# Kernel optimization log

Hardware: AMD Instinct MI355X
Metric: run time of the kernel (lower is better)

The kernel has to match this reference:

```python
import jax, jax.numpy as jnp
import numpy as np

N, C, H, W = 32, 512, 56, 56
L, CT, HEAD, GROUPS = 64, 512, 16, 16
SIZE, POS_DIM = 14, 49  # PosEncoder(size=14, num_downsample=1) -> 14^2 // 4 = 49


def setup_inputs() -> dict:
    key = jax.random.key(0)
    ks = jax.random.split(key, 8)
    return {
        "feature": jax.random.normal(ks[0], (N, C, H, W), jnp.float32),
        "w_tc": jax.random.normal(ks[1], (L, C), jnp.float32) * 0.02,
        "b_tc": jnp.zeros((L,), jnp.float32),
        "w_val": jax.random.normal(ks[2], (GROUPS, CT // GROUPS, C // GROUPS), jnp.float32) * 0.02,
        "b_val": jnp.zeros((CT,), jnp.float32),
        "w_ds3": jax.random.normal(ks[3], (1, 1, 3, 3), jnp.float32) * 0.1,
        "b_ds3": jnp.zeros((1,), jnp.float32),
        "w_ds1": jax.random.normal(ks[4], (1, 1), jnp.float32) * 0.1,
        "b_ds1": jnp.zeros((1,), jnp.float32),
        "w_pos": jax.random.normal(ks[5], (POS_DIM, POS_DIM), jnp.float32) * 0.02,
        "b_pos": jnp.zeros((POS_DIM,), jnp.float32),
        "w_tok": jax.random.normal(ks[6], (CT, CT + POS_DIM), jnp.float32) * 0.02,
        "b_tok": jnp.zeros((CT,), jnp.float32),
    }


def reference(feature, w_tc, b_tc, w_val, b_val, w_ds3, b_ds3, w_ds1, b_ds1,
              w_pos, b_pos, w_tok, b_tok):
    n, c, h, w = feature.shape
    hw = h * w
    # --- static token coefficients: 1x1 conv C->L, scale, softmax over HW ---
    tc = jnp.einsum('nchw,lc->nlhw', feature, w_tc) + b_tc[None, :, None, None]
    tc = tc.reshape(n, 1, L, hw).transpose(0, 1, 3, 2) / np.sqrt(c)  # (N,1,HW,L)
    tc = jax.nn.softmax(tc, axis=2)
    # --- grouped 1x1 conv value: C -> CT (groups=16) ---
    fg = feature.reshape(n, GROUPS, c // GROUPS, hw)
    val = jnp.einsum('ngci,gdc->ngdi', fg, w_val).reshape(n, CT, hw) + b_val[None, :, None]
    val = val.reshape(n, HEAD, CT // HEAD, hw)
    # --- token aggregation: (N,h,CT/h,HW) @ (N,1,HW,L) -> (N,CT,L) ---
    tokens = jnp.matmul(val, tc).reshape(n, CT, -1)
    # --- PosEncoder: view coef maps as images, nearest-resize to 14x14 ---
    pc = tc.reshape(n * L, 1, h, w)  # torch .view memory reinterpretation
    ih = (jnp.arange(SIZE) * h) // SIZE
    iw = (jnp.arange(SIZE) * w) // SIZE
    pc = pc[:, :, ih][:, :, :, iw]  # (N*L,1,14,14) nearest interpolate
    # conv3x3 stride 2 pad 1: 14 -> 7
    pc = jax.lax.conv_general_dilated(pc, w_ds3, (2, 2), ((1, 1), (1, 1))) + b_ds3[None, :, None, None]
    # conv1x1 (1->1)
    pc = jnp.einsum('nchw,dc->ndhw', pc, w_ds1) + b_ds1[None, :, None, None]
    pc = pc.reshape(n, L, POS_DIM).transpose(0, 2, 1)  # (N,49,L)
    pos = jnp.einsum('ncl,dc->ndl', pc, w_pos) + b_pos[None, :, None]
    # --- concat + final 1x1 conv1d (CT+49 -> CT) ---
    tokens = jnp.concatenate([tokens, pos], axis=1)
    tokens = jnp.einsum('ncl,dc->ndl', tokens, w_tok) + b_tok[None, :, None]
    return tokens  # (N, CT, L)
```

## Files before the change

### kernel.cpp

```cpp
#include <hip/hip_runtime.h>
#include <cstddef>
#include <cstdint>

namespace {

constexpr int kN = 32;
constexpr int kC = 512;
constexpr int kHW = 3136;
constexpr int kL = 64;
constexpr int kCT = 512;
constexpr int kTok = 561;
constexpr int kKcat = 576;

typedef float fx4 __attribute__((ext_vector_type(4)));
typedef float f32x4 __attribute__((ext_vector_type(4)));
typedef short short8 __attribute__((ext_vector_type(8)));
typedef unsigned int u32x2 __attribute__((ext_vector_type(2)));

static __device__ inline unsigned pack_bf16(float a, float b) {
  unsigned ua = __builtin_bit_cast(unsigned, a) + 0x8000u;
  unsigned ub = __builtin_bit_cast(unsigned, b) + 0x8000u;
  return __builtin_amdgcn_perm(ub, ua, 0x07060302u);
}

__global__ __launch_bounds__(256) void build_wcat_kernel(
    const float* __restrict__ w_tok, const float* __restrict__ w_val,
    float* __restrict__ wcat) {
  int idx = blockIdx.x * 256 + threadIdx.x;
  if (idx >= kCT * kKcat) return;
  int d = idx / kKcat;
  int c = idx - d * kKcat;
  float v = 0.f;
  if (c < kCT) {
    int g = c >> 5, k = c & 31;
    const float* wt = w_tok + (size_t)d * kTok + g * 32;
    const float* wv = w_val + g * 1024 + k;
    float s = 0.f;
#pragma unroll
    for (int dp = 0; dp < 32; ++dp) s += wt[dp] * wv[dp * 32];
    v = s;
  } else if (c < kTok) {
    v = w_tok[(size_t)d * kTok + c];
  }
  wcat[idx] = v;
}

__global__ __launch_bounds__(256) void build_cst_kernel(
    const float* __restrict__ w_tok, const float* __restrict__ b_val,
    const float* __restrict__ b_tok, float* __restrict__ cst) {
  int d = blockIdx.x * 256 + threadIdx.x;
  if (d >= kCT) return;
  float s = b_tok[d];
  for (int c = 0; c < kCT; ++c) s += w_tok[(size_t)d * kTok + c] * b_val[c];
  cst[d] = s;
}

__global__ __launch_bounds__(256) void zero_pad_kernel(float* __restrict__ bcat) {
  int i = blockIdx.x * 256 + threadIdx.x;
  const int tot = kN * kL * (kKcat - kTok);
  if (i >= tot) return;
  int n = i / (kL * 15);
  int r = i - n * (kL * 15);
  int l = r / 15;
  int k = kTok + (r - l * 15);
  bcat[(size_t)n * kL * kKcat + (size_t)l * kKcat + k] = 0.f;
}

__global__ __launch_bounds__(256) void tc_gemm_kernel(
    const float* __restrict__ feat, const float* __restrict__ w_tc,
    const float* __restrict__ b_tc, float* __restrict__ tcT) {
  const int n = blockIdx.y;
  const int pb = blockIdx.x * 256;
  const int tid = threadIdx.x;
  const int wave = tid >> 6, lane = tid & 63;
  const int quad = lane >> 4, l16 = lane & 15;
  __shared__ unsigned short As[64][72];
  __shared__ unsigned short Bs[256][72];
  __shared__ float bsm[64];
  if (tid < 64) bsm[tid] = b_tc[tid];

  f32x4 acc[4][4];
#pragma unroll
  for (int i = 0; i < 4; ++i)
#pragma unroll
    for (int j = 0; j < 4; ++j) acc[i][j] = (f32x4){0.f, 0.f, 0.f, 0.f};

  const float* fb = feat + (size_t)n * kC * kHW;
  const int al = tid & 63, akg = (tid >> 6) * 16;
  const int bc4 = (tid & 15) * 4, bpl0 = (tid >> 4) * 4;

  for (int c0 = 0; c0 < kC; c0 += 64) {
    const float* asrc = w_tc + (size_t)al * kC + c0 + akg;
#pragma unroll
    for (int u = 0; u < 4; ++u) {
      fx4 v = *(const fx4*)(asrc + u * 4);
      u32x2 w = {pack_bf16(v[0], v[1]), pack_bf16(v[2], v[3])};
      *(u32x2*)&As[al][akg + u * 4] = w;
    }
#pragma unroll
    for (int pass = 0; pass < 4; ++pass) {
      int pl = bpl0 + pass * 64;
      int pe = pb + pl;
      pe = pe < 3132 ? pe : 3132;
      fx4 v0 = *(const fx4*)(fb + (size_t)(c0 + bc4 + 0) * kHW + pe);
      fx4 v1 = *(const fx4*)(fb + (size_t)(c0 + bc4 + 1) * kHW + pe);
      fx4 v2 = *(const fx4*)(fb + (size_t)(c0 + bc4 + 2) * kHW + pe);
      fx4 v3 = *(const fx4*)(fb + (size_t)(c0 + bc4 + 3) * kHW + pe);
#pragma unroll
      for (int j = 0; j < 4; ++j) {
        u32x2 w = {pack_bf16(v0[j], v1[j]), pack_bf16(v2[j], v3[j])};
        *(u32x2*)&Bs[pl + j][bc4] = w;
      }
    }
    __syncthreads();
#pragma unroll
    for (int ks = 0; ks < 2; ++ks) {
      short8 a[4], b[4];
#pragma unroll
      for (int i = 0; i < 4; ++i)
        a[i] = *(const short8*)&As[i * 16 + l16][ks * 32 + quad * 8];
#pragma unroll
      for (int j = 0; j < 4; ++j)
        b[j] = *(const short8*)&Bs[wave * 64 + j * 16 + l16][ks * 32 + quad * 8];
#pragma unroll
      for (int i = 0; i < 4; ++i)
#pragma unroll
        for (int j = 0; j < 4; ++j)
          acc[i][j] = __builtin_amdgcn_mfma_f32_16x16x32_bf16(a[i], b[j], acc[i][j], 0, 0, 0);
    }
    __syncthreads();
  }

  const float inv = 0.04419417382415922f;
  float* ob = tcT + (size_t)n * kL * kHW;
#pragma unroll
  for (int ti = 0; ti < 4; ++ti) {
#pragma unroll
    for (int tj = 0; tj < 4; ++tj) {
      int pg = pb + wave * 64 + tj * 16 + l16;
      if (pg < kHW) {
#pragma unroll
        for (int r = 0; r < 4; ++r) {
          int l = ti * 16 + quad * 4 + r;
          ob[(size_t)l * kHW + pg] = (acc[ti][tj][r] + bsm[l]) * inv;
        }
      }
    }
  }
}

__global__ __launch_bounds__(256) void softmax_stats_kernel(
    const float* __restrict__ tcT, float* __restrict__ mArr,
    float* __restrict__ invArr) {
  const int row = blockIdx.x * 4 + (threadIdx.x >> 6);
  const int lane = threadIdx.x & 63;
  const float* src = tcT + (size_t)row * kHW + lane * 4;
  fx4 x[13];
#pragma unroll
  for (int i = 0; i < 12; ++i) x[i] = *(const fx4*)(src + i * 256);
  if (lane < 16)
    x[12] = *(const fx4*)(src + 3072);
  else
    x[12] = (fx4){-1e30f, -1e30f, -1e30f, -1e30f};
  float m = -1e30f;
#pragma unroll
  for (int i = 0; i < 13; ++i)
    m = fmaxf(m, fmaxf(fmaxf(x[i][0], x[i][1]), fmaxf(x[i][2], x[i][3])));
#pragma unroll
  for (int off = 32; off >= 1; off >>= 1) m = fmaxf(m, __shfl_xor(m, off));
  float s = 0.f;
#pragma unroll
  for (int i = 0; i < 13; ++i) {
    s += __expf(x[i][0] - m) + __expf(x[i][1] - m) + __expf(x[i][2] - m) +
         __expf(x[i][3] - m);
  }
#pragma unroll
  for (int off = 32; off >= 1; off >>= 1) s += __shfl_xor(s, off);
  if (lane == 0) {
    mArr[row] = m;
    invArr[row] = 1.f / s;
  }
}

__global__ __launch_bounds__(256) void m_gemm_kernel(
    const float* __restrict__ feat, const float* __restrict__ tcT,
    const float* __restrict__ mArr, const float* __restrict__ invArr,
    float* __restrict__ part, int klen) {
  const int cb = blockIdx.x * 256;
  const int n = blockIdx.y;
  const int s = blockIdx.z;
  const int p0s = s * klen;
  const int tid = threadIdx.x;
  const int wave = tid >> 6, lane = tid & 63;
  const int quad = lane >> 4, l16 = lane & 15;
  __shared__ unsigned short As[64][72];
  __shared__ unsigned short Bs[256][72];

  const int al = tid & 63, akg = (tid >> 6) * 16;
  const float sm = mArr[n * 64 + al];
  const float si = invArr[n * 64 + al];

  f32x4 acc[4][4];
#pragma unroll
  for (int i = 0; i < 4; ++i)
#pragma unroll
    for (int j = 0; j < 4; ++j) acc[i][j] = (f32x4){0.f, 0.f, 0.f, 0.f};

  const float* tb = tcT + (size_t)(n * 64 + al) * kHW;
  const float* fb = feat + (size_t)n * kC * kHW;
  const int bkg = (tid >> 6) * 16, bcr = tid & 63;

  for (int p0 = p0s; p0 < p0s + klen; p0 += 64) {
#pragma unroll
    for (int u = 0; u < 4; ++u) {
      fx4 v = *(const fx4*)(tb + p0 + akg + u * 4);
      float e0 = __expf(v[0] - sm) * si;
      float e1 = __expf(v[1] - sm) * si;
      float e2 = __expf(v[2] - sm) * si;
      float e3 = __expf(v[3] - sm) * si;
      u32x2 w = {pack_bf16(e0, e1), pack_bf16(e2, e3)};
      *(u32x2*)&As[al][akg + u * 4] = w;
    }
#pragma unroll
    for (int pass = 0; pass < 4; ++pass) {
      int c = cb + pass * 64 + bcr;
      const float* src = fb + (size_t)c * kHW + p0 + bkg;
#pragma unroll
      for (int u = 0; u < 4; ++u) {
        fx4 v = *(const fx4*)(src + u * 4);
        u32x2 w = {pack_bf16(v[0], v[1]), pack_bf16(v[2], v[3])};
        *(u32x2*)&Bs[pass * 64 + bcr][bkg + u * 4] = w;
      }
    }
    __syncthreads();
#pragma unroll
    for (int ks = 0; ks < 2; ++ks) {
      short8 a[4], b[4];
#pragma unroll
      for (int i = 0; i < 4; ++i)
        a[i] = *(const short8*)&As[i * 16 + l16][ks * 32 + quad * 8];
#pragma unroll
      for (int j = 0; j < 4; ++j)
        b[j] = *(const short8*)&Bs[wave * 64 + j * 16 + l16][ks * 32 + quad * 8];
#pragma unroll
      for (int i = 0; i < 4; ++i)
#pragma unroll
        for (int j = 0; j < 4; ++j)
          acc[i][j] = __builtin_amdgcn_mfma_f32_16x16x32_bf16(a[i], b[j], acc[i][j], 0, 0, 0);
    }
    __syncthreads();
  }

  float* ob = part + (size_t)(s * kN + n) * kL * kCT;
#pragma unroll
  for (int ti = 0; ti < 4; ++ti) {
#pragma unroll
    for (int tj = 0; tj < 4; ++tj) {
      int cg = cb + wave * 64 + tj * 16 + l16;
#pragma unroll
      for (int r = 0; r < 4; ++r) {
        int l = ti * 16 + quad * 4 + r;
        ob[(size_t)l * kCT + cg] = acc[ti][tj][r];
      }
    }
  }
}

__global__ __launch_bounds__(256) void reduce_m_kernel(
    const float* __restrict__ part, float* __restrict__ bcat, int ksplit) {
  int i = blockIdx.x * 256 + threadIdx.x;
  if (i >= kN * kL * kCT) return;
  int n = i >> 15;
  int r = i & 32767;
  int l = r >> 9;
  int c = r & 511;
  float s = 0.f;
  for (int ss = 0; ss < ksplit; ++ss)
    s += part[(size_t)ss * kN * kL * kCT + i];
  bcat[(size_t)n * kL * kKcat + (size_t)l * kKcat + c] = s;
}

__global__ __launch_bounds__(256) void pos_conv_kernel(
    const float* __restrict__ tcT, const float* __restrict__ mArr,
    const float* __restrict__ invArr, const float* __restrict__ w3,
    const float* __restrict__ b3, const float* __restrict__ w1,
    const float* __restrict__ b1, float* __restrict__ pcl) {
  int idx = blockIdx.x * 256 + threadIdx.x;
  if (idx >= kN * kL * 49) return;
  int n = idx / (kL * 49);
  int r = idx - n * (kL * 49);
  int lp = r / 49;
  int o = r - lp * 49;
  int y = o / 7, x = o - y * 7;
  const float* tb = tcT + (size_t)n * kL * kHW;
  const float* mB = mArr + n * 64;
  const float* iB = invArr + n * 64;
  float a = 0.f;
#pragma unroll
  for (int dy = 0; dy < 3; ++dy) {
    int i = 2 * y - 1 + dy;
    if (i < 0 || i >= 14) continue;
#pragma unroll
    for (int dx = 0; dx < 3; ++dx) {
      int j = 2 * x - 1 + dx;
      if (j < 0 || j >= 14) continue;
      int t = 224 * i + 4 * j;
      int lsm = t & 63;
      int p = lp * 49 + (t >> 6);
      float raw = tb[(size_t)lsm * kHW + p];
      a += w3[dy * 3 + dx] * (__expf(raw - mB[lsm]) * iB[lsm]);
    }
  }
  pcl[idx] = (a + b3[0]) * w1[0] + b1[0];
}

__global__ __launch_bounds__(256) void pos_out_kernel(
    const float* __restrict__ pcl, const float* __restrict__ wp,
    const float* __restrict__ bp, float* __restrict__ bcat) {
  const int n = blockIdx.x;
  __shared__ float t[64 * 49];
  for (int i = threadIdx.x; i < 64 * 49; i += 256)
    t[i] = pcl[(size_t)n * 64 * 49 + i];
  __syncthreads();
  for (int o = threadIdx.x; o < 64 * 49; o += 256) {
    int l = o / 49, d = o - l * 49;
    float s = bp[d];
#pragma unroll 7
    for (int q = 0; q < 49; ++q) s += wp[d * 49 + q] * t[l * 49 + q];
    bcat[(size_t)n * kL * kKcat + (size_t)l * kKcat + kCT + d] = s;
  }
}

__global__ __launch_bounds__(256) void out_gemm_kernel(
    const float* __restrict__ wcat, const float* __restrict__ bcat,
    const float* __restrict__ cst, float* __restrict__ out) {
  const int db = blockIdx.x * 128;
  const int n = blockIdx.y;
  const int tid = threadIdx.x;
  const int wave = tid >> 6, lane = tid & 63;
  const int quad = lane >> 4, l16 = lane & 15;
  __shared__ unsigned short As[128][72];
  __shared__ unsigned short Bs[64][72];
  __shared__ float csm[128];
  if (tid < 128) csm[tid] = cst[db + tid];

  f32x4 acc[2][4];
#pragma unroll
  for (int i = 0; i < 2; ++i)
#pragma unroll
    for (int j = 0; j < 4; ++j) acc[i][j] = (f32x4){0.f, 0.f, 0.f, 0.f};

  const int ad = tid & 127, akg = (tid >> 7) * 32;
  const int bl = tid & 63, bkg = (tid >> 6) * 16;
  const float* ab = wcat + (size_t)(db + ad) * kKcat + akg;
  const float* bb = bcat + (size_t)n * kL * kKcat + (size_t)bl * kKcat + bkg;

  for (int k0 = 0; k0 < kKcat; k0 += 64) {
#pragma unroll
    for (int u = 0; u < 8; ++u) {
      fx4 v = *(const fx4*)(ab + k0 + u * 4);
      u32x2 w = {pack_bf16(v[0], v[1]), pack_bf16(v[2], v[3])};
      *(u32x2*)&As[ad][akg + u * 4] = w;
    }
#pragma unroll
    for (int u = 0; u < 4; ++u) {
      fx4 v = *(const fx4*)(bb + k0 + u * 4);
      u32x2 w = {pack_bf16(v[0], v[1]), pack_bf16(v[2], v[3])};
      *(u32x2*)&Bs[bl][bkg + u * 4] = w;
    }
    __syncthreads();
#pragma unroll
    for (int ks = 0; ks < 2; ++ks) {
      short8 a[2], b[4];
#pragma unroll
      for (int i = 0; i < 2; ++i)
        a[i] = *(const short8*)&As[wave * 32 + i * 16 + l16][ks * 32 + quad * 8];
#pragma unroll
      for (int j = 0; j < 4; ++j)
        b[j] = *(const short8*)&Bs[j * 16 + l16][ks * 32 + quad * 8];
#pragma unroll
      for (int i = 0; i < 2; ++i)
#pragma unroll
        for (int j = 0; j < 4; ++j)
          acc[i][j] = __builtin_amdgcn_mfma_f32_16x16x32_bf16(a[i], b[j], acc[i][j], 0, 0, 0);
    }
    __syncthreads();
  }

  float* ob = out + (size_t)n * kCT * kL;
#pragma unroll
  for (int ti = 0; ti < 2; ++ti) {
#pragma unroll
    for (int tj = 0; tj < 4; ++tj) {
      int lg = tj * 16 + l16;
#pragma unroll
      for (int r = 0; r < 4; ++r) {
        int dl = wave * 32 + ti * 16 + quad * 4 + r;
        ob[(size_t)(db + dl) * kL + lg] = acc[ti][tj][r] + csm[dl];
      }
    }
  }
}

}

extern "C" void kernel_launch(void* const* d_in, const int* in_sizes, int n_in,
                              void* d_out, int out_size, void* d_ws,
                              size_t ws_size, hipStream_t stream) {
  (void)in_sizes; (void)n_in; (void)out_size;
  const float* feat  = (const float*)d_in[0];
  const float* w_tc  = (const float*)d_in[1];
  const float* b_tc  = (const float*)d_in[2];
  const float* w_val = (const float*)d_in[3];
  const float* b_val = (const float*)d_in[4];
  const float* w_ds3 = (const float*)d_in[5];
  const float* b_ds3 = (const float*)d_in[6];
  const float* w_ds1 = (const float*)d_in[7];
  const float* b_ds1 = (const float*)d_in[8];
  const float* w_pos = (const float*)d_in[9];
  const float* b_pos = (const float*)d_in[10];
  const float* w_tok = (const float*)d_in[11];
  const float* b_tok = (const float*)d_in[12];
  float* out = (float*)d_out;

  float* ws = (float*)d_ws;
  size_t off = 0;
  float* tcT = ws + off;    off += (size_t)kN * kL * kHW;
  float* bcat = ws + off;   off += (size_t)kN * kL * kKcat;
  float* wcat = ws + off;   off += (size_t)kCT * kKcat;
  float* cst = ws + off;    off += kCT;
  float* mArr = ws + off;   off += kN * 64;
  float* invArr = ws + off; off += kN * 64;
  float* pcl = ws + off;    off += (size_t)kN * kL * 49;
  int ksplit = 7;
  if (ws_size < (off + (size_t)7 * kN * kL * kCT) * sizeof(float)) ksplit = 1;
  float* part = ws + off;

  build_wcat_kernel<<<(kCT * kKcat + 255) / 256, 256, 0, stream>>>(w_tok, w_val, wcat);
  build_cst_kernel<<<2, 256, 0, stream>>>(w_tok, b_val, b_tok, cst);
  zero_pad_kernel<<<(kN * kL * 15 + 255) / 256, 256, 0, stream>>>(bcat);
  tc_gemm_kernel<<<dim3(13, kN), 256, 0, stream>>>(feat, w_tc, b_tc, tcT);
  softmax_stats_kernel<<<kN * kL / 4, 256, 0, stream>>>(tcT, mArr, invArr);
  m_gemm_kernel<<<dim3(2, kN, ksplit), 256, 0, stream>>>(
      feat, tcT, mArr, invArr, part, kHW / ksplit);
  reduce_m_kernel<<<(kN * kL * kCT + 255) / 256, 256, 0, stream>>>(part, bcat, ksplit);
  pos_conv_kernel<<<(kN * kL * 49 + 255) / 256, 256, 0, stream>>>(
      tcT, mArr, invArr, w_ds3, b_ds3, w_ds1, b_ds1, pcl);
  pos_out_kernel<<<kN, 256, 0, stream>>>(pcl, w_pos, b_pos, bcat);
  out_gemm_kernel<<<dim3(4, kN), 256, 0, stream>>>(wcat, bcat, cst, out);
}
```

Before: 448.1 us.

## Emit bf16 copy of feature in tc_gemm and read it in m_gemm

```diff
diff --git a/kernel.cpp b/kernel.cpp
--- a/kernel.cpp
+++ b/kernel.cpp
@@ -16,6 +16,7 @@
 typedef float f32x4 __attribute__((ext_vector_type(4)));
 typedef short short8 __attribute__((ext_vector_type(8)));
 typedef unsigned int u32x2 __attribute__((ext_vector_type(2)));
+typedef unsigned int u32x4 __attribute__((ext_vector_type(4)));
 
 static __device__ inline unsigned pack_bf16(float a, float b) {
   unsigned ua = __builtin_bit_cast(unsigned, a) + 0x8000u;
@@ -55,20 +56,10 @@
   cst[d] = s;
 }
 
-__global__ __launch_bounds__(256) void zero_pad_kernel(float* __restrict__ bcat) {
-  int i = blockIdx.x * 256 + threadIdx.x;
-  const int tot = kN * kL * (kKcat - kTok);
-  if (i >= tot) return;
-  int n = i / (kL * 15);
-  int r = i - n * (kL * 15);
-  int l = r / 15;
-  int k = kTok + (r - l * 15);
-  bcat[(size_t)n * kL * kKcat + (size_t)l * kKcat + k] = 0.f;
-}
-
 __global__ __launch_bounds__(256) void tc_gemm_kernel(
     const float* __restrict__ feat, const float* __restrict__ w_tc,
-    const float* __restrict__ b_tc, float* __restrict__ tcT) {
+    const float* __restrict__ b_tc, float* __restrict__ tcT,
+    unsigned short* __restrict__ featB) {
   const int n = blockIdx.y;
   const int pb = blockIdx.x * 256;
   const int tid = threadIdx.x;
@@ -86,6 +77,7 @@
     for (int j = 0; j < 4; ++j) acc[i][j] = (f32x4){0.f, 0.f, 0.f, 0.f};
 
   const float* fb = feat + (size_t)n * kC * kHW;
+  unsigned short* fBo = featB + (size_t)n * kC * kHW;
   const int al = tid & 63, akg = (tid >> 6) * 16;
   const int bc4 = (tid & 15) * 4, bpl0 = (tid >> 4) * 4;
 
@@ -106,6 +98,14 @@
       fx4 v1 = *(const fx4*)(fb + (size_t)(c0 + bc4 + 1) * kHW + pe);
       fx4 v2 = *(const fx4*)(fb + (size_t)(c0 + bc4 + 2) * kHW + pe);
       fx4 v3 = *(const fx4*)(fb + (size_t)(c0 + bc4 + 3) * kHW + pe);
+      u32x2 r0 = {pack_bf16(v0[0], v0[1]), pack_bf16(v0[2], v0[3])};
+      u32x2 r1 = {pack_bf16(v1[0], v1[1]), pack_bf16(v1[2], v1[3])};
+      u32x2 r2 = {pack_bf16(v2[0], v2[1]), pack_bf16(v2[2], v2[3])};
+      u32x2 r3 = {pack_bf16(v3[0], v3[1]), pack_bf16(v3[2], v3[3])};
+      *(u32x2*)(fBo + (size_t)(c0 + bc4 + 0) * kHW + pe) = r0;
+      *(u32x2*)(fBo + (size_t)(c0 + bc4 + 1) * kHW + pe) = r1;
+      *(u32x2*)(fBo + (size_t)(c0 + bc4 + 2) * kHW + pe) = r2;
+      *(u32x2*)(fBo + (size_t)(c0 + bc4 + 3) * kHW + pe) = r3;
 #pragma unroll
       for (int j = 0; j < 4; ++j) {
         u32x2 w = {pack_bf16(v0[j], v1[j]), pack_bf16(v2[j], v3[j])};
@@ -183,7 +183,7 @@
 }
 
 __global__ __launch_bounds__(256) void m_gemm_kernel(
-    const float* __restrict__ feat, const float* __restrict__ tcT,
+    const unsigned short* __restrict__ featB, const float* __restrict__ tcT,
     const float* __restrict__ mArr, const float* __restrict__ invArr,
     float* __restrict__ part, int klen) {
   const int cb = blockIdx.x * 256;
@@ -207,7 +207,7 @@
     for (int j = 0; j < 4; ++j) acc[i][j] = (f32x4){0.f, 0.f, 0.f, 0.f};
 
   const float* tb = tcT + (size_t)(n * 64 + al) * kHW;
-  const float* fb = feat + (size_t)n * kC * kHW;
+  const unsigned short* fBo = featB + (size_t)n * kC * kHW;
   const int bkg = (tid >> 6) * 16, bcr = tid & 63;
 
   for (int p0 = p0s; p0 < p0s + klen; p0 += 64) {
@@ -224,13 +224,11 @@
 #pragma unroll
     for (int pass = 0; pass < 4; ++pass) {
       int c = cb + pass * 64 + bcr;
-      const float* src = fb + (size_t)c * kHW + p0 + bkg;
-#pragma unroll
-      for (int u = 0; u < 4; ++u) {
-        fx4 v = *(const fx4*)(src + u * 4);
-        u32x2 w = {pack_bf16(v[0], v[1]), pack_bf16(v[2], v[3])};
-        *(u32x2*)&Bs[pass * 64 + bcr][bkg + u * 4] = w;
-      }
+      const unsigned short* src = fBo + (size_t)c * kHW + p0 + bkg;
+      u32x4 v0 = *(const u32x4*)src;
+      u32x4 v1 = *(const u32x4*)(src + 8);
+      *(u32x4*)&Bs[pass * 64 + bcr][bkg] = v0;
+      *(u32x4*)&Bs[pass * 64 + bcr][bkg + 8] = v1;
     }
     __syncthreads();
 #pragma unroll
@@ -322,11 +320,14 @@
   for (int i = threadIdx.x; i < 64 * 49; i += 256)
     t[i] = pcl[(size_t)n * 64 * 49 + i];
   __syncthreads();
-  for (int o = threadIdx.x; o < 64 * 49; o += 256) {
-    int l = o / 49, d = o - l * 49;
-    float s = bp[d];
+  for (int o = threadIdx.x; o < 64 * 64; o += 256) {
+    int l = o >> 6, d = o & 63;
+    float s = 0.f;
+    if (d < 49) {
+      s = bp[d];
 #pragma unroll 7
-    for (int q = 0; q < 49; ++q) s += wp[d * 49 + q] * t[l * 49 + q];
+      for (int q = 0; q < 49; ++q) s += wp[d * 49 + q] * t[l * 49 + q];
+    }
     bcat[(size_t)n * kL * kKcat + (size_t)l * kKcat + kCT + d] = s;
   }
 }
@@ -432,17 +433,18 @@
   float* mArr = ws + off;   off += kN * 64;
   float* invArr = ws + off; off += kN * 64;
   float* pcl = ws + off;    off += (size_t)kN * kL * 49;
+  unsigned short* featB = (unsigned short*)(ws + off);
+  off += (size_t)kN * kC * kHW / 2;
   int ksplit = 7;
   if (ws_size < (off + (size_t)7 * kN * kL * kCT) * sizeof(float)) ksplit = 1;
   float* part = ws + off;
 
   build_wcat_kernel<<<(kCT * kKcat + 255) / 256, 256, 0, stream>>>(w_tok, w_val, wcat);
   build_cst_kernel<<<2, 256, 0, stream>>>(w_tok, b_val, b_tok, cst);
-  zero_pad_kernel<<<(kN * kL * 15 + 255) / 256, 256, 0, stream>>>(bcat);
-  tc_gemm_kernel<<<dim3(13, kN), 256, 0, stream>>>(feat, w_tc, b_tc, tcT);
+  tc_gemm_kernel<<<dim3(13, kN), 256, 0, stream>>>(feat, w_tc, b_tc, tcT, featB);
   softmax_stats_kernel<<<kN * kL / 4, 256, 0, stream>>>(tcT, mArr, invArr);
   m_gemm_kernel<<<dim3(2, kN, ksplit), 256, 0, stream>>>(
-      feat, tcT, mArr, invArr, part, kHW / ksplit);
+      featB, tcT, mArr, invArr, part, kHW / ksplit);
   reduce_m_kernel<<<(kN * kL * kCT + 255) / 256, 256, 0, stream>>>(part, bcat, ksplit);
   pos_conv_kernel<<<(kN * kL * 49 + 255) / 256, 256, 0, stream>>>(
       tcT, mArr, invArr, w_ds3, b_ds3, w_ds1, b_ds1, pcl);
```

Measured after the change: 485.7 us. 1.08x slower.
